# Performance work log

Hardware: AMD Instinct MI355X
Metric: run time of the kernel (lower is better)

Reference implementation:

```python
import jax, jax.numpy as jnp
import numpy as np


def setup_inputs() -> dict:
    key = jax.random.key(0)
    k1, k2 = jax.random.split(key)
    x = jax.random.normal(k1, (8192, 4096), dtype=jnp.float32)
    W = jax.random.normal(k2, (4096, 4096), dtype=jnp.float32)
    return {"x": x, "W": W}


def reference(x, W):
    # y = x @ sign(W); sign maps 0 -> 0, matching tf.math.sign
    return jnp.matmul(x, jnp.sign(W))
```

## Files before the change

kernel.cpp:

```cpp
#include <hip/hip_runtime.h>

typedef unsigned short u16;
typedef __bf16 bf16x8 __attribute__((ext_vector_type(8)));
typedef float f32x4 __attribute__((ext_vector_type(4)));
typedef unsigned short u16x4 __attribute__((ext_vector_type(4)));

__device__ __forceinline__ u16 f2bf(float f) {
  unsigned int u = __builtin_bit_cast(unsigned int, f);
  u += 0x7FFFu + ((u >> 16) & 1u);
  return (u16)(u >> 16);
}

__device__ __forceinline__ u16 signbf(float f) {
  return f > 0.f ? (u16)0x3F80u : (f < 0.f ? (u16)0xBF80u : (u16)0u);
}

__device__ __forceinline__ void lds_load16(const void* g, void* l) {
  __builtin_amdgcn_global_load_lds(
      (const __attribute__((address_space(1))) unsigned int*)g,
      (__attribute__((address_space(3))) unsigned int*)l, 16, 0, 0);
}

__global__ void cvt_x(const float* __restrict__ x, u16* __restrict__ xb, long long nv) {
  long long stride = (long long)gridDim.x * blockDim.x;
  for (long long i = (long long)blockIdx.x * blockDim.x + threadIdx.x; i < nv; i += stride) {
    float4 v = reinterpret_cast<const float4*>(x)[i];
    u16x4 o = { f2bf(v.x), f2bf(v.y), f2bf(v.z), f2bf(v.w) };
    reinterpret_cast<u16x4*>(xb)[i] = o;
  }
}

__global__ void cvt_w(const float* __restrict__ W, u16* __restrict__ wt, int K, int N) {
  __shared__ u16 t[32][34];
  int n0 = blockIdx.x * 32, k0 = blockIdx.y * 32;
  int tx = threadIdx.x, ty = threadIdx.y;
#pragma unroll
  for (int r = 0; r < 4; ++r) {
    int k = ty + r * 8;
    t[k][tx] = signbf(W[(long long)(k0 + k) * N + n0 + tx]);
  }
  __syncthreads();
#pragma unroll
  for (int r = 0; r < 4; ++r) {
    int n = ty + r * 8;
    wt[(long long)(n0 + n) * K + k0 + tx] = t[tx][n];
  }
}

template <int XPRE>
__global__ __launch_bounds__(256) void gemm_sign(
    const float* __restrict__ xf, const u16* __restrict__ xb,
    const u16* __restrict__ wt, float* __restrict__ y, int M, int N, int K) {
  __shared__ u16 As[128 * 64];
  __shared__ u16 Bs[128 * 64];

  const int tid = threadIdx.x;
  const int lane = tid & 63;
  const int w = tid >> 6;

  const int nbx = N >> 7;
  const int bx = blockIdx.x % nbx;
  const int by = blockIdx.x / nbx;
  const long long bm0 = (long long)by << 7;
  const long long bn0 = (long long)bx << 7;

  const int wm = (w >> 1) << 6;
  const int wn = (w & 1) << 6;
  const int lr = lane & 15;
  const int lg = lane >> 4;

  f32x4 acc[4][4];
#pragma unroll
  for (int i = 0; i < 4; ++i)
#pragma unroll
    for (int j = 0; j < 4; ++j)
      acc[i][j] = f32x4{0.f, 0.f, 0.f, 0.f};

  const int srow = w * 32 + (lane >> 3);
  const int scol = (lane & 7) * 8;
  const u16* aglb = XPRE ? (xb + (bm0 + srow) * K + scol) : nullptr;
  const u16* bglb = wt + (bn0 + srow) * K + scol;
  u16* AsW = &As[(w * 32) * 64];
  u16* BsW = &Bs[(w * 32) * 64];

  const int xrow = tid >> 4;
  const int xcol = (tid & 15) * 4;
  const float* xglb = XPRE ? nullptr : (xf + (bm0 + xrow) * K + xcol);

  const int nkt = K >> 6;
  for (int kt = 0; kt < nkt; ++kt) {
    if (kt) __syncthreads();
    const int kofs = kt * 64;
    if (XPRE) {
#pragma unroll
      for (int it = 0; it < 4; ++it)
        lds_load16(aglb + (long long)it * 8 * K + kofs, AsW + it * 8 * 64);
    } else {
#pragma unroll
      for (int i = 0; i < 8; ++i) {
        float4 v = *reinterpret_cast<const float4*>(xglb + (long long)i * 16 * K + kofs);
        u16x4 o = { f2bf(v.x), f2bf(v.y), f2bf(v.z), f2bf(v.w) };
        *reinterpret_cast<u16x4*>(&As[(xrow + i * 16) * 64 + xcol]) = o;
      }
    }
#pragma unroll
    for (int it = 0; it < 4; ++it)
      lds_load16(bglb + (long long)it * 8 * K + kofs, BsW + it * 8 * 64);

    __syncthreads();

    const u16* Ab = &As[(wm + lr) * 64 + lg * 8];
    const u16* Bb = &Bs[(wn + lr) * 64 + lg * 8];
#pragma unroll
    for (int ks = 0; ks < 2; ++ks) {
      bf16x8 a[4], b[4];
#pragma unroll
      for (int mi = 0; mi < 4; ++mi)
        a[mi] = *reinterpret_cast<const bf16x8*>(Ab + mi * 16 * 64 + ks * 32);
#pragma unroll
      for (int ni = 0; ni < 4; ++ni)
        b[ni] = *reinterpret_cast<const bf16x8*>(Bb + ni * 16 * 64 + ks * 32);
#pragma unroll
      for (int mi = 0; mi < 4; ++mi)
#pragma unroll
        for (int ni = 0; ni < 4; ++ni)
          acc[mi][ni] = __builtin_amdgcn_mfma_f32_16x16x32_bf16(a[mi], b[ni], acc[mi][ni], 0, 0, 0);
    }
  }

  float* yb = y + (bm0 + wm + lg * 4) * N + bn0 + wn + lr;
#pragma unroll
  for (int mi = 0; mi < 4; ++mi)
#pragma unroll
    for (int r = 0; r < 4; ++r)
#pragma unroll
      for (int ni = 0; ni < 4; ++ni)
        yb[(long long)(mi * 16 + r) * N + ni * 16] = acc[mi][ni][r];
}

__global__ void naive_gemm(const float* __restrict__ x, const float* __restrict__ W,
                           float* __restrict__ y, int M, int N, int K) {
  long long i = (long long)blockIdx.x * blockDim.x + threadIdx.x;
  if (i >= (long long)M * N) return;
  int m = (int)(i / N), n = (int)(i % N);
  const float* xr = x + (long long)m * K;
  float acc = 0.f;
  for (int k = 0; k < K; ++k) {
    float wv = W[(long long)k * N + n];
    acc += (wv > 0.f ? xr[k] : (wv < 0.f ? -xr[k] : 0.f));
  }
  y[i] = acc;
}

extern "C" void kernel_launch(void* const* d_in, const int* in_sizes, int n_in,
                              void* d_out, int out_size, void* d_ws, size_t ws_size,
                              hipStream_t stream) {
  const float* x = (const float*)d_in[0];
  const float* W = (const float*)d_in[1];
  float* y = (float*)d_out;
  const int K = 4096, N = 4096;
  const int M = in_sizes[0] / K;

  const size_t xb_bytes = (size_t)M * K * sizeof(u16);
  const size_t wt_bytes = (size_t)K * N * sizeof(u16);

  if (ws_size < wt_bytes) {
    long long tot = (long long)M * N;
    int blocks = (int)((tot + 255) / 256);
    naive_gemm<<<blocks, 256, 0, stream>>>(x, W, y, M, N, K);
    return;
  }

  const bool xpre = ws_size >= xb_bytes + wt_bytes;
  u16* xb = nullptr;
  u16* wt;
  if (xpre) { xb = (u16*)d_ws; wt = xb + (size_t)M * K; }
  else      { wt = (u16*)d_ws; }

  dim3 wgrid(N / 32, K / 32), wblk(32, 8);
  cvt_w<<<wgrid, wblk, 0, stream>>>(W, wt, K, N);
  if (xpre)
    cvt_x<<<2048, 256, 0, stream>>>(x, xb, (long long)M * K / 4);

  dim3 ggrid((M / 128) * (N / 128)), gblk(256);
  if (xpre) gemm_sign<1><<<ggrid, gblk, 0, stream>>>(x, xb, wt, y, M, N, K);
  else      gemm_sign<0><<<ggrid, gblk, 0, stream>>>(x, xb, wt, y, M, N, K);
}
```

Before: 547.4 us.

## Replace GEMM with 256x256-tile 8-wave double-buffered pipelined kernel

Swaps the 128x128 single-buffered bf16 MFMA GEMM for a 256x256 tile kernel with 512 threads and 128KB of dynamic LDS, double-buffered across k-tiles. Global-to-LDS loads for later k-steps are interleaved with MFMA phases, using vmcnt waits, s_setprio and an XOR swizzle to reduce LDS bank conflicts. Workgroups are also remapped across XCDs for L2 locality. This aims to hide memory latency and raise MFMA utilisation. The cost is heavy LDS use that allows only one workgroup per CU, more register pressure, and a fallback path that is stricter about shapes.

```diff
diff --git a/kernel.cpp b/kernel.cpp
--- a/kernel.cpp
+++ b/kernel.cpp
@@ -47,95 +47,112 @@
   }
 }
 
-template <int XPRE>
-__global__ __launch_bounds__(256) void gemm_sign(
-    const float* __restrict__ xf, const u16* __restrict__ xb,
-    const u16* __restrict__ wt, float* __restrict__ y, int M, int N, int K) {
-  __shared__ u16 As[128 * 64];
-  __shared__ u16 Bs[128 * 64];
+__global__ __launch_bounds__(512, 2) void gemm8p(
+    const u16* __restrict__ xb, const u16* __restrict__ wt,
+    float* __restrict__ y, int M, int N, int K) {
+  extern __shared__ u16 lds[];
 
   const int tid = threadIdx.x;
   const int lane = tid & 63;
   const int w = tid >> 6;
 
-  const int nbx = N >> 7;
-  const int bx = blockIdx.x % nbx;
-  const int by = blockIdx.x / nbx;
-  const long long bm0 = (long long)by << 7;
-  const long long bn0 = (long long)bx << 7;
-
-  const int wm = (w >> 1) << 6;
-  const int wn = (w & 1) << 6;
-  const int lr = lane & 15;
-  const int lg = lane >> 4;
-
-  f32x4 acc[4][4];
-#pragma unroll
-  for (int i = 0; i < 4; ++i)
+  const int nbx = N >> 8;
+  int wg = blockIdx.x;
+  const int nwg = gridDim.x;
+  if ((nwg & 7) == 0) wg = (wg & 7) * (nwg >> 3) + (wg >> 3);
+  const int by = wg / nbx, bx = wg % nbx;
+  const long long bm0 = (long long)by << 8;
+  const long long bn0 = (long long)bx << 8;
+
+  const int lr = lane & 15, lg = lane >> 4;
+  const int wm0 = (w >> 2) * 128;
+  const int wn0 = (w & 3) * 64;
+
+  const int rswz = (lr >> 1) & 3;
+  const int aoff = (wm0 + lr) * 32 + ((lg ^ rswz) << 3);
+  const int boff = (wn0 + lr) * 32 + ((lg ^ rswz) << 3);
+
+  const int schunk = (lane & 3) ^ ((lane >> 3) & 3);
+  const int srow = lane >> 2;
+  const u16* asrc = xb + (bm0 + w * 32 + srow) * (long long)K + schunk * 8;
+  const u16* bsrc = wt + (bn0 + w * 32 + srow) * (long long)K + schunk * 8;
+  u16* aldsw = lds + w * 1024;
+  u16* bldsw = lds + 32768 + w * 1024;
+
+  f32x4 acc[8][4];
+#pragma unroll
+  for (int i = 0; i < 8; ++i)
 #pragma unroll
     for (int j = 0; j < 4; ++j)
       acc[i][j] = f32x4{0.f, 0.f, 0.f, 0.f};
 
-  const int srow = w * 32 + (lane >> 3);
-  const int scol = (lane & 7) * 8;
-  const u16* aglb = XPRE ? (xb + (bm0 + srow) * K + scol) : nullptr;
-  const u16* bglb = wt + (bn0 + srow) * K + scol;
-  u16* AsW = &As[(w * 32) * 64];
-  u16* BsW = &Bs[(w * 32) * 64];
-
-  const int xrow = tid >> 4;
-  const int xcol = (tid & 15) * 4;
-  const float* xglb = XPRE ? nullptr : (xf + (bm0 + xrow) * K + xcol);
-
   const int nkt = K >> 6;
-  for (int kt = 0; kt < nkt; ++kt) {
-    if (kt) __syncthreads();
-    const int kofs = kt * 64;
-    if (XPRE) {
-#pragma unroll
-      for (int it = 0; it < 4; ++it)
-        lds_load16(aglb + (long long)it * 8 * K + kofs, AsW + it * 8 * 64);
-    } else {
-#pragma unroll
-      for (int i = 0; i < 8; ++i) {
-        float4 v = *reinterpret_cast<const float4*>(xglb + (long long)i * 16 * K + kofs);
-        u16x4 o = { f2bf(v.x), f2bf(v.y), f2bf(v.z), f2bf(v.w) };
-        *reinterpret_cast<u16x4*>(&As[(xrow + i * 16) * 64 + xcol]) = o;
-      }
-    }
-#pragma unroll
-    for (int it = 0; it < 4; ++it)
-      lds_load16(bglb + (long long)it * 8 * K + kofs, BsW + it * 8 * 64);
-
-    __syncthreads();
-
-    const u16* Ab = &As[(wm + lr) * 64 + lg * 8];
-    const u16* Bb = &Bs[(wn + lr) * 64 + lg * 8];
-#pragma unroll
-    for (int ks = 0; ks < 2; ++ks) {
-      bf16x8 a[4], b[4];
-#pragma unroll
-      for (int mi = 0; mi < 4; ++mi)
-        a[mi] = *reinterpret_cast<const bf16x8*>(Ab + mi * 16 * 64 + ks * 32);
-#pragma unroll
-      for (int ni = 0; ni < 4; ++ni)
-        b[ni] = *reinterpret_cast<const bf16x8*>(Bb + ni * 16 * 64 + ks * 32);
-#pragma unroll
-      for (int mi = 0; mi < 4; ++mi)
-#pragma unroll
-        for (int ni = 0; ni < 4; ++ni)
-          acc[mi][ni] = __builtin_amdgcn_mfma_f32_16x16x32_bf16(a[mi], b[ni], acc[mi][ni], 0, 0, 0);
-    }
-  }
-
-  float* yb = y + (bm0 + wm + lg * 4) * N + bn0 + wn + lr;
-#pragma unroll
-  for (int mi = 0; mi < 4; ++mi)
+
+  auto stageA = [&](int t, int ks) {
+    const u16* s = asrc + t * 64 + ks * 32;
+    u16* d = aldsw + (t & 1) * 16384 + ks * 8192;
+#pragma unroll
+    for (int it = 0; it < 2; ++it)
+      lds_load16(s + (long long)it * 16 * K, d + it * 512);
+  };
+  auto stageB = [&](int t, int ks) {
+    const u16* s = bsrc + t * 64 + ks * 32;
+    u16* d = bldsw + (t & 1) * 16384 + ks * 8192;
+#pragma unroll
+    for (int it = 0; it < 2; ++it)
+      lds_load16(s + (long long)it * 16 * K, d + it * 512);
+  };
+
+  stageA(0, 0); stageB(0, 0); stageA(0, 1); stageB(0, 1);
+  stageA(1, 0); stageB(1, 0);
+  asm volatile("s_waitcnt vmcnt(4)" ::: "memory");
+  __builtin_amdgcn_s_barrier();
+
+  bf16x8 a[8];
+
+#define PHASE(qks, qnp, RDA, STAGE_STMT)                                        \
+  {                                                                             \
+    const int lbase = (t & 1) * 16384 + (qks)*8192;                             \
+    if (RDA) {                                                                  \
+      _Pragma("unroll") for (int mf = 0; mf < 8; ++mf)                          \
+          a[mf] = *(const bf16x8*)&lds[lbase + aoff + mf * 512];                \
+    }                                                                           \
+    bf16x8 b0 = *(const bf16x8*)&lds[32768 + lbase + boff + ((qnp)*2) * 512];   \
+    bf16x8 b1 = *(const bf16x8*)&lds[32768 + lbase + boff + ((qnp)*2 + 1) * 512]; \
+    STAGE_STMT;                                                                 \
+    __builtin_amdgcn_s_barrier();                                               \
+    __builtin_amdgcn_s_setprio(1);                                              \
+    _Pragma("unroll") for (int mf = 0; mf < 8; ++mf) {                          \
+      acc[mf][(qnp)*2] = __builtin_amdgcn_mfma_f32_16x16x32_bf16(               \
+          a[mf], b0, acc[mf][(qnp)*2], 0, 0, 0);                                \
+      acc[mf][(qnp)*2 + 1] = __builtin_amdgcn_mfma_f32_16x16x32_bf16(           \
+          a[mf], b1, acc[mf][(qnp)*2 + 1], 0, 0, 0);                            \
+    }                                                                           \
+    __builtin_amdgcn_s_setprio(0);                                              \
+  }
+
+  for (int t = 0; t < nkt; ++t) {
+    PHASE(0, 0, true,  { if (t + 1 < nkt) stageA(t + 1, 1); })
+    __builtin_amdgcn_s_barrier();
+    PHASE(0, 1, false, { if (t + 1 < nkt) stageB(t + 1, 1); })
+    __builtin_amdgcn_s_barrier();
+    PHASE(1, 0, true,  { if (t + 2 < nkt) stageA(t + 2, 0); })
+    __builtin_amdgcn_s_barrier();
+    PHASE(1, 1, false, { if (t + 2 < nkt) stageB(t + 2, 0); })
+    if (t == nkt - 2)     asm volatile("s_waitcnt vmcnt(0)" ::: "memory");
+    else if (t < nkt - 2) asm volatile("s_waitcnt vmcnt(4)" ::: "memory");
+    __builtin_amdgcn_s_barrier();
+  }
+#undef PHASE
+
+  float* yb = y + (bm0 + wm0 + lg * 4) * N + bn0 + wn0 + lr;
+#pragma unroll
+  for (int mf = 0; mf < 8; ++mf)
 #pragma unroll
     for (int r = 0; r < 4; ++r)
 #pragma unroll
-      for (int ni = 0; ni < 4; ++ni)
-        yb[(long long)(mi * 16 + r) * N + ni * 16] = acc[mi][ni][r];
+      for (int nf = 0; nf < 4; ++nf)
+        yb[(long long)(mf * 16 + r) * N + nf * 16] = acc[mf][nf][r];
 }
 
 __global__ void naive_gemm(const float* __restrict__ x, const float* __restrict__ W,
@@ -164,25 +181,21 @@
   const size_t xb_bytes = (size_t)M * K * sizeof(u16);
   const size_t wt_bytes = (size_t)K * N * sizeof(u16);
 
-  if (ws_size < wt_bytes) {
+  if (ws_size < xb_bytes + wt_bytes || (M & 255) || (N & 255) || (K & 127)) {
     long long tot = (long long)M * N;
-    int blocks = (int)((tot + 255) / 256);
-    naive_gemm<<<blocks, 256, 0, stream>>>(x, W, y, M, N, K);
+    naive_gemm<<<(int)((tot + 255) / 256), 256, 0, stream>>>(x, W, y, M, N, K);
     return;
   }
 
-  const bool xpre = ws_size >= xb_bytes + wt_bytes;
-  u16* xb = nullptr;
-  u16* wt;
-  if (xpre) { xb = (u16*)d_ws; wt = xb + (size_t)M * K; }
-  else      { wt = (u16*)d_ws; }
+  u16* xb = (u16*)d_ws;
+  u16* wt = xb + (size_t)M * K;
 
   dim3 wgrid(N / 32, K / 32), wblk(32, 8);
   cvt_w<<<wgrid, wblk, 0, stream>>>(W, wt, K, N);
-  if (xpre)
-    cvt_x<<<2048, 256, 0, stream>>>(x, xb, (long long)M * K / 4);
-
-  dim3 ggrid((M / 128) * (N / 128)), gblk(256);
-  if (xpre) gemm_sign<1><<<ggrid, gblk, 0, stream>>>(x, xb, wt, y, M, N, K);
-  else      gemm_sign<0><<<ggrid, gblk, 0, stream>>>(x, xb, wt, y, M, N, K);
-}
+  cvt_x<<<4096, 256, 0, stream>>>(x, xb, (long long)M * K / 4);
+
+  hipFuncSetAttribute(reinterpret_cast<const void*>(gemm8p),
+                      hipFuncAttributeMaxDynamicSharedMemorySize, 131072);
+  dim3 ggrid((M / 256) * (N / 256));
+  gemm8p<<<ggrid, dim3(512), 131072, stream>>>(xb, wt, y, M, N, K);
+}
```

After: 502.8 us. 1.09x faster.
